# Kernel tuning notes

Measured on AMD Instinct MI355X. Metric: run time of the kernel, lower is better.

Reference implementation:

```python
import jax, jax.numpy as jnp
import numpy as np

SEQ, BATCH, IN, HID, LAYERS = 512, 32, 1024, 1024, 4


def setup_inputs() -> dict:
    key = jax.random.key(0)
    ks = jax.random.split(key, 5)
    s = 1.0 / np.sqrt(HID)  # torch-style U(-1/sqrt(H), 1/sqrt(H)) scale via scaled normal
    x = jax.random.normal(ks[0], (SEQ, BATCH, IN), dtype=jnp.float32)
    W_ih = jax.random.uniform(ks[1], (LAYERS, 4 * HID, IN), jnp.float32, -s, s)
    W_hh = jax.random.uniform(ks[2], (LAYERS, 4 * HID, HID), jnp.float32, -s, s)
    b_ih = jax.random.uniform(ks[3], (LAYERS, 4 * HID), jnp.float32, -s, s)
    b_hh = jax.random.uniform(ks[4], (LAYERS, 4 * HID), jnp.float32, -s, s)
    return {"x": x, "W_ih": W_ih, "W_hh": W_hh, "b_ih": b_ih, "b_hh": b_hh}


def _run_layer(inp, wih, whh, bih, bhh):
    # inp: [S, B, D]; wih: [4H, D]; whh: [4H, H]
    H = whh.shape[-1]
    B = inp.shape[1]
    # Precompute input projections for all timesteps in one big GEMM.
    x_gates = jnp.einsum('sbd,gd->sbg', inp, wih) + bih + bhh  # [S, B, 4H]

    def step(carry, xg_t):
        h, c = carry
        g = xg_t + h @ whh.T  # [B, 4H]
        i, f, gg, o = jnp.split(g, 4, axis=-1)  # torch gate order: i, f, g, o
        c_new = jax.nn.sigmoid(f) * c + jax.nn.sigmoid(i) * jnp.tanh(gg)
        h_new = jax.nn.sigmoid(o) * jnp.tanh(c_new)
        return (h_new, c_new), h_new

    h0 = jnp.zeros((B, H), inp.dtype)
    (h_last, c_last), ys = jax.lax.scan(step, (h0, h0), x_gates)
    return ys, h_last, c_last


def reference(x, W_ih, W_hh, b_ih, b_hh):
    out = x
    hs, cs = [], []
    for l in range(W_ih.shape[0]):  # fixed small layer count
        out, h, c = _run_layer(out, W_ih[l], W_hh[l], b_ih[l], b_hh[l])
        hs.append(h)
        cs.append(c)
    # x_outs: [S, B, H]; hs/cs: [L, B, H] (concatenation of per-layer final states)
    return out, jnp.stack(hs, axis=0), jnp.stack(cs, axis=0)
```

## Files before the change

kernel.cpp:

```cpp
#include <hip/hip_runtime.h>
#include <stdint.h>


#define SEQ    512
#define BATCH  32
#define HID    1024
#define G4     4096
#define LAYERS 4

typedef unsigned short u16;
typedef unsigned int u32;
typedef unsigned long long u64;
typedef __attribute__((ext_vector_type(8))) short bf8;
typedef __attribute__((ext_vector_type(4))) float f4;

__device__ __forceinline__ u16 f2bf(float f) {
  uint32_t u = __float_as_uint(f);
  u += 0x7FFFu + ((u >> 16) & 1u);
  return (u16)(u >> 16);
}
__device__ __forceinline__ float bf2f(u16 h) {
  return __uint_as_float(((uint32_t)h) << 16);
}
__device__ __forceinline__ float sigf(float x) { return 1.f / (1.f + __expf(-x)); }

__device__ __forceinline__ bf8 ld_bf8_sc(const u16* p) {
  union { u64 q[2]; bf8 v; } u;
  const u64* qp = (const u64*)p;
  u.q[0] = __hip_atomic_load(qp,     __ATOMIC_RELAXED, __HIP_MEMORY_SCOPE_AGENT);
  u.q[1] = __hip_atomic_load(qp + 1, __ATOMIC_RELAXED, __HIP_MEMORY_SCOPE_AGENT);
  return u.v;
}

__global__ void cvt_split_kernel(const float* __restrict__ in, u16* __restrict__ hi,
                                 u16* __restrict__ lo, int n4) {
  int i = blockIdx.x * 256 + threadIdx.x;
  if (i >= n4) return;
  float4 v = reinterpret_cast<const float4*>(in)[i];
  ushort4 h, l;
  h.x = f2bf(v.x); l.x = f2bf(v.x - bf2f(h.x));
  h.y = f2bf(v.y); l.y = f2bf(v.y - bf2f(h.y));
  h.z = f2bf(v.z); l.z = f2bf(v.z - bf2f(h.z));
  h.w = f2bf(v.w); l.w = f2bf(v.w - bf2f(h.w));
  reinterpret_cast<ushort4*>(hi)[i] = h;
  reinterpret_cast<ushort4*>(lo)[i] = l;
}

__global__ void bias_comb_kernel(const float* __restrict__ a, const float* __restrict__ b,
                                 float* __restrict__ o, int n) {
  int i = blockIdx.x * 256 + threadIdx.x;
  if (i < n) o[i] = a[i] + b[i];
}

__launch_bounds__(256)
__global__ void gemm_xproj(const u16* __restrict__ Ah, const u16* __restrict__ Al,
                           const u16* __restrict__ Bh, const u16* __restrict__ Bl,
                           const float* __restrict__ bias, float* __restrict__ C) {
  __shared__ u16 Ash[128 * 32];
  __shared__ u16 Asl[128 * 32];
  __shared__ u16 Bsh[128 * 32];
  __shared__ u16 Bsl[128 * 32];
  const int tid  = threadIdx.x;
  const int lane = tid & 63;
  const int w    = tid >> 6;
  const int wm   = (w >> 1) * 64, wn = (w & 1) * 64;
  const int m0   = blockIdx.x * 128, n0 = blockIdx.y * 128;
  const int fr   = lane & 15;
  const int fk   = (lane >> 4) * 8;
  const f4 fz = {0.f, 0.f, 0.f, 0.f};
  f4 acc[4][4];
#pragma unroll
  for (int i = 0; i < 4; ++i)
#pragma unroll
    for (int j = 0; j < 4; ++j) acc[i][j] = fz;

  for (int kt = 0; kt < 1024; kt += 32) {
    __syncthreads();
#pragma unroll
    for (int i = 0; i < 2; ++i) {
      const int e   = (i * 256 + tid) * 8;
      const int row = e >> 5, kc = e & 31;
      const int ldsbase = (i * 256 + (tid & 192)) * 8;
      const size_t goffA = (size_t)(m0 + row) * 1024 + kt + kc;
      const size_t goffB = (size_t)(n0 + row) * 1024 + kt + kc;
      __builtin_amdgcn_global_load_lds(
          (const __attribute__((address_space(1))) void*)(Ah + goffA),
          (__attribute__((address_space(3))) void*)(Ash + ldsbase), 16, 0, 0);
      __builtin_amdgcn_global_load_lds(
          (const __attribute__((address_space(1))) void*)(Al + goffA),
          (__attribute__((address_space(3))) void*)(Asl + ldsbase), 16, 0, 0);
      __builtin_amdgcn_global_load_lds(
          (const __attribute__((address_space(1))) void*)(Bh + goffB),
          (__attribute__((address_space(3))) void*)(Bsh + ldsbase), 16, 0, 0);
      __builtin_amdgcn_global_load_lds(
          (const __attribute__((address_space(1))) void*)(Bl + goffB),
          (__attribute__((address_space(3))) void*)(Bsl + ldsbase), 16, 0, 0);
    }
    __syncthreads();
    bf8 ah[4], al[4], bh[4], bl[4];
#pragma unroll
    for (int f = 0; f < 4; ++f) {
      ah[f] = *reinterpret_cast<const bf8*>(Ash + (wm + f * 16 + fr) * 32 + fk);
      al[f] = *reinterpret_cast<const bf8*>(Asl + (wm + f * 16 + fr) * 32 + fk);
      bh[f] = *reinterpret_cast<const bf8*>(Bsh + (wn + f * 16 + fr) * 32 + fk);
      bl[f] = *reinterpret_cast<const bf8*>(Bsl + (wn + f * 16 + fr) * 32 + fk);
    }
#pragma unroll
    for (int i = 0; i < 4; ++i)
#pragma unroll
      for (int j = 0; j < 4; ++j) {
        acc[i][j] = __builtin_amdgcn_mfma_f32_16x16x32_bf16(ah[i], bh[j], acc[i][j], 0, 0, 0);
        acc[i][j] = __builtin_amdgcn_mfma_f32_16x16x32_bf16(ah[i], bl[j], acc[i][j], 0, 0, 0);
        acc[i][j] = __builtin_amdgcn_mfma_f32_16x16x32_bf16(al[i], bh[j], acc[i][j], 0, 0, 0);
      }
  }
  const int cr0 = (lane >> 4) * 4;
#pragma unroll
  for (int i = 0; i < 4; ++i)
#pragma unroll
    for (int j = 0; j < 4; ++j)
#pragma unroll
      for (int q = 0; q < 4; ++q) {
        const int rr = m0 + wm + i * 16 + cr0 + q;
        const int cc = n0 + wn + j * 16 + fr;
        C[(size_t)rr * 4096 + cc] = acc[i][j][q] + bias[cc];
      }
}

#define WLD   1032
#define HPP_Q 32768
#define WBYTES (32 * WLD * 2)
#define SSMEM (2 * WBYTES + 16384)

__launch_bounds__(256, 1)
__global__ void lstm_scan(const float* __restrict__ gates,
                          const u16* __restrict__ Whh_hi,
                          const u16* __restrict__ Whh_lo,
                          u16* __restrict__ h_pp,
                          float* __restrict__ c_glob,
                          float* __restrict__ hseq_f,
                          float* __restrict__ hs_out,
                          float* __restrict__ cs_out,
                          int* __restrict__ slots,
                          int* __restrict__ go_rep,
                          int t0, int tag0, int nsteps, int is_last) {
  extern __shared__ char smem[];
  u16*   Wh  = (u16*)smem;
  u16*   Wl  = (u16*)(smem + WBYTES);
  float* red = (float*)(smem + 2 * WBYTES);

  const int bid = blockIdx.x;
  const int ug  = bid;
  const int tid = threadIdx.x, lane = tid & 63, w = tid >> 6;

  {
    const int n  = tid & 31;
    const int ch = tid >> 5;
    const size_t grow = (size_t)((n >> 3) * 1024 + ug * 8 + (n & 7));
    const u16* sh = Whh_hi + grow * 1024 + ch * 128;
    const u16* sl = Whh_lo + grow * 1024 + ch * 128;
    u16* dh = Wh + n * WLD + ch * 128;
    u16* dl = Wl + n * WLD + ch * 128;
#pragma unroll
    for (int it = 0; it < 16; ++it) {
      *reinterpret_cast<bf8*>(dh + it * 8) = *reinterpret_cast<const bf8*>(sh + it * 8);
      *reinterpret_cast<bf8*>(dl + it * 8) = *reinterpret_cast<const bf8*>(sl + it * 8);
    }
  }

  float c0 = 0.f, c1 = 0.f;
  int b = 0, up = 0, u0 = 0;
  if (tid < 128) {
    b = tid >> 2; up = tid & 3;
    u0 = ug * 8 + up * 2;
    c0 = c_glob[b * 1024 + u0];
    c1 = c_glob[b * 1024 + u0 + 1];
  }
  __syncthreads();

  const int fr = lane & 15, q4 = lane >> 4;
  const int khq = w;
  const int aeo0 = fr * 8;
  const int aeo1 = (16 + fr) * 8;
  const int brow0 = fr * WLD;
  const int brow1 = (16 + fr) * WLD;
  const int bcol0 = khq * 256 + q4 * 8;

  const f4 fz = {0.f, 0.f, 0.f, 0.f};

  for (int s = 0; s < nsteps; ++s) {
    const int t = t0 + s;
    float2 gp0, gp1, gp2, gp3;
    if (tid < 128) {
      const float* gr = gates + (size_t)(s * 32 + b) * 4096 + u0;
      gp0 = *(const float2*)(gr);
      gp1 = *(const float2*)(gr + 1024);
      gp2 = *(const float2*)(gr + 2048);
      gp3 = *(const float2*)(gr + 3072);
    }
    {
      const u16* hh = h_pp + (size_t)((t & 1) * 2 + 0) * HPP_Q;
      const u16* hl = h_pp + (size_t)((t & 1) * 2 + 1) * HPP_Q;
      f4 a00 = fz, a01 = fz, a10 = fz, a11 = fz;
#pragma unroll
      for (int kc8 = 0; kc8 < 32; kc8 += 4) {
        const int ab = (khq * 32 + kc8 + q4) * 256;
        bf8 avh0 = ld_bf8_sc(hh + ab + aeo0);
        bf8 avl0 = ld_bf8_sc(hl + ab + aeo0);
        bf8 avh1 = ld_bf8_sc(hh + ab + aeo1);
        bf8 avl1 = ld_bf8_sc(hl + ab + aeo1);
        const int bc = bcol0 + kc8 * 8;
        bf8 bvh0 = *reinterpret_cast<const bf8*>(Wh + brow0 + bc);
        bf8 bvl0 = *reinterpret_cast<const bf8*>(Wl + brow0 + bc);
        bf8 bvh1 = *reinterpret_cast<const bf8*>(Wh + brow1 + bc);
        bf8 bvl1 = *reinterpret_cast<const bf8*>(Wl + brow1 + bc);
        a00 = __builtin_amdgcn_mfma_f32_16x16x32_bf16(avh0, bvh0, a00, 0, 0, 0);
        a00 = __builtin_amdgcn_mfma_f32_16x16x32_bf16(avh0, bvl0, a00, 0, 0, 0);
        a00 = __builtin_amdgcn_mfma_f32_16x16x32_bf16(avl0, bvh0, a00, 0, 0, 0);
        a01 = __builtin_amdgcn_mfma_f32_16x16x32_bf16(avh0, bvh1, a01, 0, 0, 0);
        a01 = __builtin_amdgcn_mfma_f32_16x16x32_bf16(avh0, bvl1, a01, 0, 0, 0);
        a01 = __builtin_amdgcn_mfma_f32_16x16x32_bf16(avl0, bvh1, a01, 0, 0, 0);
        a10 = __builtin_amdgcn_mfma_f32_16x16x32_bf16(avh1, bvh0, a10, 0, 0, 0);
        a10 = __builtin_amdgcn_mfma_f32_16x16x32_bf16(avh1, bvl0, a10, 0, 0, 0);
        a10 = __builtin_amdgcn_mfma_f32_16x16x32_bf16(avl1, bvh0, a10, 0, 0, 0);
        a11 = __builtin_amdgcn_mfma_f32_16x16x32_bf16(avh1, bvh1, a11, 0, 0, 0);
        a11 = __builtin_amdgcn_mfma_f32_16x16x32_bf16(avh1, bvl1, a11, 0, 0, 0);
        a11 = __builtin_amdgcn_mfma_f32_16x16x32_bf16(avl1, bvh1, a11, 0, 0, 0);
      }
      float* r00 = red + (khq * 2 + 0) * 512 + fr * 16 + q4 * 4;
      float* r01 = r00 + 256;
      float* r10 = red + (khq * 2 + 1) * 512 + fr * 16 + q4 * 4;
      float* r11 = r10 + 256;
#pragma unroll
      for (int q = 0; q < 4; ++q) {
        r00[q] = a00[q]; r01[q] = a01[q]; r10[q] = a10[q]; r11[q] = a11[q];
      }
    }
    __syncthreads();
    if (tid < 128) {
      const int bl = b & 15, bmt = b >> 4;
      float g00, g01, g02, g03, g10, g11, g12, g13;
      {
        const int nb0 = (up * 2) * 16 + bl;
        float s0, s1, s2, s3;
#pragma unroll
        for (int j = 0; j < 2; ++j) {
          const int nb = nb0 + j * 16;
          s0 = s1 = s2 = s3 = 0.f;
#pragma unroll
          for (int kq = 0; kq < 4; ++kq) {
            const float* rb = red + (kq * 2 + bmt) * 512 + nb;
            s0 += rb[0 * 128];
            s1 += rb[1 * 128];
            s2 += rb[2 * 128];
            s3 += rb[3 * 128];
          }
          if (j == 0) { g00 = s0 + gp0.x; g01 = s1 + gp1.x; g02 = s2 + gp2.x; g03 = s3 + gp3.x; }
          else        { g10 = s0 + gp0.y; g11 = s1 + gp1.y; g12 = s2 + gp2.y; g13 = s3 + gp3.y; }
        }
      }
      const float i0 = sigf(g00), f0 = sigf(g01), z0 = tanhf(g02), o0 = sigf(g03);
      c0 = f0 * c0 + i0 * z0;
      const float h0 = o0 * tanhf(c0);
      const float i1 = sigf(g10), f1 = sigf(g11), z1 = tanhf(g12), o1 = sigf(g13);
      c1 = f1 * c1 + i1 * z1;
      const float h1 = o1 * tanhf(c1);
      const u64 hv = ((u64)__float_as_uint(h1) << 32) | (u64)__float_as_uint(h0);
      __hip_atomic_store((u64*)(hseq_f + ((size_t)t * 32 + b) * 1024 + u0), hv,
                         __ATOMIC_RELAXED, __HIP_MEMORY_SCOPE_AGENT);
      const u16 h0h = f2bf(h0), h0l = f2bf(h0 - bf2f(h0h));
      const u16 h1h = f2bf(h1), h1l = f2bf(h1 - bf2f(h1h));
      const int par2 = ((t + 1) & 1) * 2;
      const int tix  = ug * 256 + b * 8 + up * 2;
      __hip_atomic_store((u32*)(h_pp + (size_t)par2 * HPP_Q + tix),
                         (u32)h0h | ((u32)h1h << 16),
                         __ATOMIC_RELAXED, __HIP_MEMORY_SCOPE_AGENT);
      __hip_atomic_store((u32*)(h_pp + (size_t)(par2 + 1) * HPP_Q + tix),
                         (u32)h0l | ((u32)h1l << 16),
                         __ATOMIC_RELAXED, __HIP_MEMORY_SCOPE_AGENT);
      if (is_last && s == nsteps - 1) {
        hs_out[b * 1024 + u0]     = h0;
        hs_out[b * 1024 + u0 + 1] = h1;
        cs_out[b * 1024 + u0]     = c0;
        cs_out[b * 1024 + u0 + 1] = c1;
      }
    }
    __syncthreads();
    const int tag = tag0 + s + 1;
    if (tid == 0)
      __hip_atomic_store(slots + bid, tag, __ATOMIC_RELEASE, __HIP_MEMORY_SCOPE_AGENT);
    if (bid == 0) {
      if (w == 0) {
        for (;;) {
          int v0 = __hip_atomic_load(slots + lane,      __ATOMIC_RELAXED, __HIP_MEMORY_SCOPE_AGENT);
          int v1 = __hip_atomic_load(slots + 64 + lane, __ATOMIC_RELAXED, __HIP_MEMORY_SCOPE_AGENT);
          if (__all(v0 >= tag && v1 >= tag)) break;
          __builtin_amdgcn_s_sleep(1);
        }
        __builtin_amdgcn_fence(__ATOMIC_ACQ_REL, "agent");
        if (lane < 32)
          __hip_atomic_store(go_rep + lane * 16, tag, __ATOMIC_RELAXED, __HIP_MEMORY_SCOPE_AGENT);
      }
    } else if (tid == 0) {
      while (__hip_atomic_load(go_rep + (bid & 31) * 16, __ATOMIC_RELAXED, __HIP_MEMORY_SCOPE_AGENT) < tag)
        __builtin_amdgcn_s_sleep(2);
    }
    __syncthreads();
  }
  if (tid < 128) {
    c_glob[b * 1024 + u0]     = c0;
    c_glob[b * 1024 + u0 + 1] = c1;
  }
}

extern "C" void kernel_launch(void* const* d_in, const int* in_sizes, int n_in,
                              void* d_out, int out_size, void* d_ws, size_t ws_size,
                              hipStream_t stream) {
  const float* x   = (const float*)d_in[0];
  const float* Wih = (const float*)d_in[1];
  const float* Whh = (const float*)d_in[2];
  const float* bih = (const float*)d_in[3];
  const float* bhh = (const float*)d_in[4];
  float* out = (float*)d_out;

  float* outh = out;
  const size_t OFF1 = (size_t)SEQ * BATCH * HID;
  const size_t OFF2 = OFF1 + (size_t)LAYERS * BATCH * HID;

  char* ws = (char*)d_ws;
  u16*   wih_hi = (u16*)ws;
  u16*   wih_lo = (u16*)(ws + (8ull  << 20));
  u16*   whh_hi = (u16*)(ws + (16ull << 20));
  u16*   whh_lo = (u16*)(ws + (24ull << 20));
  float* biasc  = (float*)(ws + (32ull << 20));
  u16*   h_pp   = (u16*)(ws + (32ull << 20) + (64ull << 10));
  float* c_glob = (float*)(ws + (32ull << 20) + (320ull << 10));
  int*   bar    = (int*)(ws + (32ull << 20) + (448ull << 10));
  char*  dynws  = ws + (33ull << 20);

  int T = 128;
  while (T > 8 && (33ull << 20) + (size_t)T * (640ull << 10) > ws_size) T >>= 1;
  const int nchunk = SEQ / T;
  u16*   xb_hi = (u16*)dynws;
  u16*   xb_lo = (u16*)(dynws + (size_t)T * BATCH * HID * sizeof(u16));
  float* gates = (float*)(dynws + (size_t)2 * T * BATCH * HID * sizeof(u16));

  hipFuncSetAttribute(reinterpret_cast<const void*>(lstm_scan),
                      hipFuncAttributeMaxDynamicSharedMemorySize, SSMEM);

  hipMemsetAsync(bar, 0, 4096, stream);
  bias_comb_kernel<<<(LAYERS * G4 + 255) / 256, 256, 0, stream>>>(bih, bhh, biasc, LAYERS * G4);

  int tag0 = 0;
  for (int l = 0; l < LAYERS; ++l) {
    cvt_split_kernel<<<G4 * HID / 4 / 256, 256, 0, stream>>>(
        Wih + (size_t)l * G4 * HID, wih_hi, wih_lo, G4 * HID / 4);
    cvt_split_kernel<<<G4 * HID / 4 / 256, 256, 0, stream>>>(
        Whh + (size_t)l * G4 * HID, whh_hi, whh_lo, G4 * HID / 4);
    hipMemsetAsync(h_pp, 0, 4 * HPP_Q * sizeof(u16), stream);
    hipMemsetAsync(c_glob, 0, BATCH * HID * sizeof(float), stream);
    for (int cch = 0; cch < nchunk; ++cch) {
      const float* asrc = (l == 0) ? (x + (size_t)cch * T * BATCH * HID)
                                   : (outh + (size_t)cch * T * BATCH * HID);
      cvt_split_kernel<<<T * BATCH * HID / 4 / 256, 256, 0, stream>>>(
          asrc, xb_hi, xb_lo, T * BATCH * HID / 4);
      gemm_xproj<<<dim3(T * BATCH / 128, 32), 256, 0, stream>>>(
          xb_hi, xb_lo, wih_hi, wih_lo, biasc + l * G4, gates);
      lstm_scan<<<128, 256, SSMEM, stream>>>(
          gates, whh_hi, whh_lo, h_pp, c_glob,
          outh,
          out + OFF1 + (size_t)l * BATCH * HID,
          out + OFF2 + (size_t)l * BATCH * HID,
          bar, bar + 128,
          cch * T, tag0, T, (cch == nchunk - 1) ? 1 : 0);
      tag0 += T;
    }
  }
  (void)in_sizes; (void)n_in; (void)out_size;
}
```

Measured before the change: 14.75 ms.

## Keep recurrent weights in registers and replace two-level grid barrier with all-to-all polling

The W_hh slice for each block now sits in VGPRs instead of LDS, which removes the per-step LDS weight reads and the large dynamic shared allocation. The grid barrier becomes a flat scheme: each wave publishes its own slot, and every wave polls all 512 slots directly, so the master-block relay through go_rep is gone. Gate inputs for the next step are prefetched during the current step, and tanhf is replaced with an exp-based approximation. The risks are higher register pressure, more polling traffic to L2 from every wave, and tanh accuracy that may drift for extreme inputs.

```diff
diff --git a/kernel.cpp b/kernel.cpp
--- a/kernel.cpp
+++ b/kernel.cpp
@@ -23,6 +23,9 @@
   return __uint_as_float(((uint32_t)h) << 16);
 }
 __device__ __forceinline__ float sigf(float x) { return 1.f / (1.f + __expf(-x)); }
+__device__ __forceinline__ float tanhfast(float x) {
+  return 1.f - 2.f / (1.f + __expf(2.f * x));
+}
 
 __device__ __forceinline__ bf8 ld_bf8_sc(const u16* p) {
   union { u64 q[2]; bf8 v; } u;
@@ -127,10 +130,7 @@
       }
 }
 
-#define WLD   1032
 #define HPP_Q 32768
-#define WBYTES (32 * WLD * 2)
-#define SSMEM (2 * WBYTES + 16384)
 
 __launch_bounds__(256, 1)
 __global__ void lstm_scan(const float* __restrict__ gates,
@@ -142,90 +142,78 @@
                           float* __restrict__ hs_out,
                           float* __restrict__ cs_out,
                           int* __restrict__ slots,
-                          int* __restrict__ go_rep,
                           int t0, int tag0, int nsteps, int is_last) {
-  extern __shared__ char smem[];
-  u16*   Wh  = (u16*)smem;
-  u16*   Wl  = (u16*)(smem + WBYTES);
-  float* red = (float*)(smem + 2 * WBYTES);
+  __shared__ float red[4096];
 
   const int bid = blockIdx.x;
   const int ug  = bid;
   const int tid = threadIdx.x, lane = tid & 63, w = tid >> 6;
 
+  const int fr = lane & 15, q4 = lane >> 4;
+  const int khq = w;
+  const int bcol0 = khq * 256 + q4 * 8;
+
+  bf8 wh0[8], wl0[8], wh1[8], wl1[8];
   {
-    const int n  = tid & 31;
-    const int ch = tid >> 5;
-    const size_t grow = (size_t)((n >> 3) * 1024 + ug * 8 + (n & 7));
-    const u16* sh = Whh_hi + grow * 1024 + ch * 128;
-    const u16* sl = Whh_lo + grow * 1024 + ch * 128;
-    u16* dh = Wh + n * WLD + ch * 128;
-    u16* dl = Wl + n * WLD + ch * 128;
-#pragma unroll
-    for (int it = 0; it < 16; ++it) {
-      *reinterpret_cast<bf8*>(dh + it * 8) = *reinterpret_cast<const bf8*>(sh + it * 8);
-      *reinterpret_cast<bf8*>(dl + it * 8) = *reinterpret_cast<const bf8*>(sl + it * 8);
+    const size_t grow0 = (size_t)((fr >> 3) * 1024 + ug * 8 + (fr & 7));
+    const size_t grow1 = grow0 + 2048;
+    const u16* bh0 = Whh_hi + grow0 * 1024 + bcol0;
+    const u16* bl0 = Whh_lo + grow0 * 1024 + bcol0;
+    const u16* bh1 = Whh_hi + grow1 * 1024 + bcol0;
+    const u16* bl1 = Whh_lo + grow1 * 1024 + bcol0;
+#pragma unroll
+    for (int i = 0; i < 8; ++i) {
+      wh0[i] = *reinterpret_cast<const bf8*>(bh0 + 32 * i);
+      wl0[i] = *reinterpret_cast<const bf8*>(bl0 + 32 * i);
+      wh1[i] = *reinterpret_cast<const bf8*>(bh1 + 32 * i);
+      wl1[i] = *reinterpret_cast<const bf8*>(bl1 + 32 * i);
     }
   }
 
   float c0 = 0.f, c1 = 0.f;
   int b = 0, up = 0, u0 = 0;
+  float2 gp0, gp1, gp2, gp3;
   if (tid < 128) {
     b = tid >> 2; up = tid & 3;
     u0 = ug * 8 + up * 2;
     c0 = c_glob[b * 1024 + u0];
     c1 = c_glob[b * 1024 + u0 + 1];
-  }
-  __syncthreads();
-
-  const int fr = lane & 15, q4 = lane >> 4;
-  const int khq = w;
+    const float* gr = gates + (size_t)b * 4096 + u0;
+    gp0 = *(const float2*)(gr);
+    gp1 = *(const float2*)(gr + 1024);
+    gp2 = *(const float2*)(gr + 2048);
+    gp3 = *(const float2*)(gr + 3072);
+  }
+
   const int aeo0 = fr * 8;
   const int aeo1 = (16 + fr) * 8;
-  const int brow0 = fr * WLD;
-  const int brow1 = (16 + fr) * WLD;
-  const int bcol0 = khq * 256 + q4 * 8;
-
   const f4 fz = {0.f, 0.f, 0.f, 0.f};
 
   for (int s = 0; s < nsteps; ++s) {
     const int t = t0 + s;
-    float2 gp0, gp1, gp2, gp3;
-    if (tid < 128) {
-      const float* gr = gates + (size_t)(s * 32 + b) * 4096 + u0;
-      gp0 = *(const float2*)(gr);
-      gp1 = *(const float2*)(gr + 1024);
-      gp2 = *(const float2*)(gr + 2048);
-      gp3 = *(const float2*)(gr + 3072);
-    }
     {
       const u16* hh = h_pp + (size_t)((t & 1) * 2 + 0) * HPP_Q;
       const u16* hl = h_pp + (size_t)((t & 1) * 2 + 1) * HPP_Q;
       f4 a00 = fz, a01 = fz, a10 = fz, a11 = fz;
 #pragma unroll
-      for (int kc8 = 0; kc8 < 32; kc8 += 4) {
-        const int ab = (khq * 32 + kc8 + q4) * 256;
+      for (int i = 0; i < 8; ++i) {
+        const int ab = (khq * 32 + 4 * i + q4) * 256;
         bf8 avh0 = ld_bf8_sc(hh + ab + aeo0);
         bf8 avl0 = ld_bf8_sc(hl + ab + aeo0);
         bf8 avh1 = ld_bf8_sc(hh + ab + aeo1);
         bf8 avl1 = ld_bf8_sc(hl + ab + aeo1);
-        const int bc = bcol0 + kc8 * 8;
-        bf8 bvh0 = *reinterpret_cast<const bf8*>(Wh + brow0 + bc);
-        bf8 bvl0 = *reinterpret_cast<const bf8*>(Wl + brow0 + bc);
-        bf8 bvh1 = *reinterpret_cast<const bf8*>(Wh + brow1 + bc);
-        bf8 bvl1 = *reinterpret_cast<const bf8*>(Wl + brow1 + bc);
-        a00 = __builtin_amdgcn_mfma_f32_16x16x32_bf16(avh0, bvh0, a00, 0, 0, 0);
-        a00 = __builtin_amdgcn_mfma_f32_16x16x32_bf16(avh0, bvl0, a00, 0, 0, 0);
-        a00 = __builtin_amdgcn_mfma_f32_16x16x32_bf16(avl0, bvh0, a00, 0, 0, 0);
-        a01 = __builtin_amdgcn_mfma_f32_16x16x32_bf16(avh0, bvh1, a01, 0, 0, 0);
-        a01 = __builtin_amdgcn_mfma_f32_16x16x32_bf16(avh0, bvl1, a01, 0, 0, 0);
-        a01 = __builtin_amdgcn_mfma_f32_16x16x32_bf16(avl0, bvh1, a01, 0, 0, 0);
-        a10 = __builtin_amdgcn_mfma_f32_16x16x32_bf16(avh1, bvh0, a10, 0, 0, 0);
-        a10 = __builtin_amdgcn_mfma_f32_16x16x32_bf16(avh1, bvl0, a10, 0, 0, 0);
-        a10 = __builtin_amdgcn_mfma_f32_16x16x32_bf16(avl1, bvh0, a10, 0, 0, 0);
-        a11 = __builtin_amdgcn_mfma_f32_16x16x32_bf16(avh1, bvh1, a11, 0, 0, 0);
-        a11 = __builtin_amdgcn_mfma_f32_16x16x32_bf16(avh1, bvl1, a11, 0, 0, 0);
-        a11 = __builtin_amdgcn_mfma_f32_16x16x32_bf16(avl1, bvh1, a11, 0, 0, 0);
+        a00 = __builtin_amdgcn_mfma_f32_16x16x32_bf16(avh0, wh0[i], a00, 0, 0, 0);
+        a00 = __builtin_amdgcn_mfma_f32_16x16x32_bf16(avh0, wl0[i], a00, 0, 0, 0);
+        a00 = __builtin_amdgcn_mfma_f32_16x16x32_bf16(avl0, wh0[i], a00, 0, 0, 0);
+        a01 = __builtin_amdgcn_mfma_f32_16x16x32_bf16(avh0, wh1[i], a01, 0, 0, 0);
+        a01 = __builtin_amdgcn_mfma_f32_16x16x32_bf16(avh0, wl1[i], a01, 0, 0, 0);
+        a01 = __builtin_amdgcn_mfma_f32_16x16x32_bf16(avl0, wh1[i], a01, 0, 0, 0);
+        a10 = __builtin_amdgcn_mfma_f32_16x16x32_bf16(avh1, wh0[i], a10, 0, 0, 0);
+        a10 = __builtin_amdgcn_mfma_f32_16x16x32_bf16(avh1, wl0[i], a10, 0, 0, 0);
+        a10 = __builtin_amdgcn_mfma_f32_16x16x32_bf16(avl1, wh0[i], a10, 0, 0, 0);
+        a11 = __builtin_amdgcn_mfma_f32_16x16x32_bf16(avh1, wh1[i], a11, 0, 0, 0);
+        a11 = __builtin_amdgcn_mfma_f32_16x16x32_bf16(avh1, wl1[i], a11, 0, 0, 0);
+        a11 = __builtin_amdgcn_mfma_f32_16x16x32_bf16(avl1, wh1[i], a11, 0, 0, 0);
       }
       float* r00 = red + (khq * 2 + 0) * 512 + fr * 16 + q4 * 4;
       float* r01 = r00 + 256;
@@ -238,6 +226,15 @@
     }
     __syncthreads();
     if (tid < 128) {
+      float2 gn0, gn1, gn2, gn3;
+      {
+        const int sp = (s + 1 < nsteps) ? s + 1 : s;
+        const float* gr = gates + (size_t)(sp * 32 + b) * 4096 + u0;
+        gn0 = *(const float2*)(gr);
+        gn1 = *(const float2*)(gr + 1024);
+        gn2 = *(const float2*)(gr + 2048);
+        gn3 = *(const float2*)(gr + 3072);
+      }
       const int bl = b & 15, bmt = b >> 4;
       float g00, g01, g02, g03, g10, g11, g12, g13;
       {
@@ -259,12 +256,12 @@
           else        { g10 = s0 + gp0.y; g11 = s1 + gp1.y; g12 = s2 + gp2.y; g13 = s3 + gp3.y; }
         }
       }
-      const float i0 = sigf(g00), f0 = sigf(g01), z0 = tanhf(g02), o0 = sigf(g03);
+      const float i0 = sigf(g00), f0 = sigf(g01), z0 = tanhfast(g02), o0 = sigf(g03);
       c0 = f0 * c0 + i0 * z0;
-      const float h0 = o0 * tanhf(c0);
-      const float i1 = sigf(g10), f1 = sigf(g11), z1 = tanhf(g12), o1 = sigf(g13);
+      const float h0 = o0 * tanhfast(c0);
+      const float i1 = sigf(g10), f1 = sigf(g11), z1 = tanhfast(g12), o1 = sigf(g13);
       c1 = f1 * c1 + i1 * z1;
-      const float h1 = o1 * tanhf(c1);
+      const float h1 = o1 * tanhfast(c1);
       const u64 hv = ((u64)__float_as_uint(h1) << 32) | (u64)__float_as_uint(h0);
       __hip_atomic_store((u64*)(hseq_f + ((size_t)t * 32 + b) * 1024 + u0), hv,
                          __ATOMIC_RELAXED, __HIP_MEMORY_SCOPE_AGENT);
@@ -284,28 +281,28 @@
         cs_out[b * 1024 + u0]     = c0;
         cs_out[b * 1024 + u0 + 1] = c1;
       }
-    }
-    __syncthreads();
-    const int tag = tag0 + s + 1;
-    if (tid == 0)
-      __hip_atomic_store(slots + bid, tag, __ATOMIC_RELEASE, __HIP_MEMORY_SCOPE_AGENT);
-    if (bid == 0) {
-      if (w == 0) {
-        for (;;) {
-          int v0 = __hip_atomic_load(slots + lane,      __ATOMIC_RELAXED, __HIP_MEMORY_SCOPE_AGENT);
-          int v1 = __hip_atomic_load(slots + 64 + lane, __ATOMIC_RELAXED, __HIP_MEMORY_SCOPE_AGENT);
-          if (__all(v0 >= tag && v1 >= tag)) break;
-          __builtin_amdgcn_s_sleep(1);
-        }
-        __builtin_amdgcn_fence(__ATOMIC_ACQ_REL, "agent");
-        if (lane < 32)
-          __hip_atomic_store(go_rep + lane * 16, tag, __ATOMIC_RELAXED, __HIP_MEMORY_SCOPE_AGENT);
-      }
-    } else if (tid == 0) {
-      while (__hip_atomic_load(go_rep + (bid & 31) * 16, __ATOMIC_RELAXED, __HIP_MEMORY_SCOPE_AGENT) < tag)
-        __builtin_amdgcn_s_sleep(2);
-    }
-    __syncthreads();
+      gp0 = gn0; gp1 = gn1; gp2 = gn2; gp3 = gn3;
+    }
+    if (s + 1 < nsteps) {
+      const int tag = tag0 + s + 1;
+      if (w < 2) asm volatile("s_waitcnt vmcnt(0)" ::: "memory");
+      if (lane == 0)
+        __hip_atomic_store(slots + bid * 4 + w, tag, __ATOMIC_RELAXED, __HIP_MEMORY_SCOPE_AGENT);
+      const u64* sl64 = (const u64*)slots;
+      for (;;) {
+        u64 v0 = __hip_atomic_load(sl64 + lane * 4 + 0, __ATOMIC_RELAXED, __HIP_MEMORY_SCOPE_AGENT);
+        u64 v1 = __hip_atomic_load(sl64 + lane * 4 + 1, __ATOMIC_RELAXED, __HIP_MEMORY_SCOPE_AGENT);
+        u64 v2 = __hip_atomic_load(sl64 + lane * 4 + 2, __ATOMIC_RELAXED, __HIP_MEMORY_SCOPE_AGENT);
+        u64 v3 = __hip_atomic_load(sl64 + lane * 4 + 3, __ATOMIC_RELAXED, __HIP_MEMORY_SCOPE_AGENT);
+        bool ok = ((int)v0 >= tag) && ((int)(v0 >> 32) >= tag)
+               && ((int)v1 >= tag) && ((int)(v1 >> 32) >= tag)
+               && ((int)v2 >= tag) && ((int)(v2 >> 32) >= tag)
+               && ((int)v3 >= tag) && ((int)(v3 >> 32) >= tag);
+        if (__all(ok)) break;
+        __builtin_amdgcn_s_sleep(1);
+      }
+      __builtin_amdgcn_sched_barrier(0);
+    }
   }
   if (tid < 128) {
     c_glob[b * 1024 + u0]     = c0;
@@ -344,9 +341,6 @@
   u16*   xb_hi = (u16*)dynws;
   u16*   xb_lo = (u16*)(dynws + (size_t)T * BATCH * HID * sizeof(u16));
   float* gates = (float*)(dynws + (size_t)2 * T * BATCH * HID * sizeof(u16));
-
-  hipFuncSetAttribute(reinterpret_cast<const void*>(lstm_scan),
-                      hipFuncAttributeMaxDynamicSharedMemorySize, SSMEM);
 
   hipMemsetAsync(bar, 0, 4096, stream);
   bias_comb_kernel<<<(LAYERS * G4 + 255) / 256, 256, 0, stream>>>(bih, bhh, biasc, LAYERS * G4);
@@ -366,12 +360,12 @@
           asrc, xb_hi, xb_lo, T * BATCH * HID / 4);
       gemm_xproj<<<dim3(T * BATCH / 128, 32), 256, 0, stream>>>(
           xb_hi, xb_lo, wih_hi, wih_lo, biasc + l * G4, gates);
-      lstm_scan<<<128, 256, SSMEM, stream>>>(
+      lstm_scan<<<128, 256, 0, stream>>>(
           gates, whh_hi, whh_lo, h_pp, c_glob,
           outh,
           out + OFF1 + (size_t)l * BATCH * HID,
           out + OFF2 + (size_t)l * BATCH * HID,
-          bar, bar + 128,
+          bar,
           cch * T, tag0, T, (cch == nchunk - 1) ? 1 : 0);
       tag0 += T;
     }
```

Result: slower. 22.79 ms (+54.6%).

## Replace centralized grid barrier with per-wave polling of producer flags

Applied to the files above, without the earlier changes.

Drops the two-stage grid barrier (all blocks report to block 0, which then broadcasts a go flag). Instead each block publishes a per-step flag in its own padded slot, and each wave spins only on the 8×4 producer blocks whose h slice it reads, right before its MFMA k-range. This aims to cut barrier round-trip latency on the sequential time loop and lets blocks drift apart slightly. Flags are now stored relaxed rather than with release ordering, and double-buffered h may be overwritten early, so there is a memory-ordering and WAR risk. Also swaps tanhf for an exp-based fast tanh and changes the LDS row padding of the weight tile.

```diff
diff --git a/kernel.cpp b/kernel.cpp
--- a/kernel.cpp
+++ b/kernel.cpp
@@ -23,6 +23,9 @@
   return __uint_as_float(((uint32_t)h) << 16);
 }
 __device__ __forceinline__ float sigf(float x) { return 1.f / (1.f + __expf(-x)); }
+__device__ __forceinline__ float tanhfast(float x) {
+  return 1.f - 2.f / (1.f + __expf(2.f * x));
+}
 
 __device__ __forceinline__ bf8 ld_bf8_sc(const u16* p) {
   union { u64 q[2]; bf8 v; } u;
@@ -127,7 +130,7 @@
       }
 }
 
-#define WLD   1032
+#define WLD   1036
 #define HPP_Q 32768
 #define WBYTES (32 * WLD * 2)
 #define SSMEM (2 * WBYTES + 16384)
@@ -142,7 +145,6 @@
                           float* __restrict__ hs_out,
                           float* __restrict__ cs_out,
                           int* __restrict__ slots,
-                          int* __restrict__ go_rep,
                           int t0, int tag0, int nsteps, int is_last) {
   extern __shared__ char smem[];
   u16*   Wh  = (u16*)smem;
@@ -185,7 +187,7 @@
   const int brow0 = fr * WLD;
   const int brow1 = (16 + fr) * WLD;
   const int bcol0 = khq * 256 + q4 * 8;
-
+  const int pbase = (khq * 32 + q4) * 16;
   const f4 fz = {0.f, 0.f, 0.f, 0.f};
 
   for (int s = 0; s < nsteps; ++s) {
@@ -197,6 +199,21 @@
       gp1 = *(const float2*)(gr + 1024);
       gp2 = *(const float2*)(gr + 2048);
       gp3 = *(const float2*)(gr + 3072);
+    }
+    {
+      const int tagS = tag0 + s;
+      for (;;) {
+        bool ok = true;
+#pragma unroll
+        for (int i = 0; i < 8; ++i) {
+          int v = __hip_atomic_load(slots + pbase + i * 64,
+                                    __ATOMIC_RELAXED, __HIP_MEMORY_SCOPE_AGENT);
+          ok &= (v >= tagS);
+        }
+        if (ok) break;
+        __builtin_amdgcn_s_sleep(1);
+      }
+      __builtin_amdgcn_sched_barrier(0);
     }
     {
       const u16* hh = h_pp + (size_t)((t & 1) * 2 + 0) * HPP_Q;
@@ -259,12 +276,12 @@
           else        { g10 = s0 + gp0.y; g11 = s1 + gp1.y; g12 = s2 + gp2.y; g13 = s3 + gp3.y; }
         }
       }
-      const float i0 = sigf(g00), f0 = sigf(g01), z0 = tanhf(g02), o0 = sigf(g03);
+      const float i0 = sigf(g00), f0 = sigf(g01), z0 = tanhfast(g02), o0 = sigf(g03);
       c0 = f0 * c0 + i0 * z0;
-      const float h0 = o0 * tanhf(c0);
-      const float i1 = sigf(g10), f1 = sigf(g11), z1 = tanhf(g12), o1 = sigf(g13);
+      const float h0 = o0 * tanhfast(c0);
+      const float i1 = sigf(g10), f1 = sigf(g11), z1 = tanhfast(g12), o1 = sigf(g13);
       c1 = f1 * c1 + i1 * z1;
-      const float h1 = o1 * tanhf(c1);
+      const float h1 = o1 * tanhfast(c1);
       const u64 hv = ((u64)__float_as_uint(h1) << 32) | (u64)__float_as_uint(h0);
       __hip_atomic_store((u64*)(hseq_f + ((size_t)t * 32 + b) * 1024 + u0), hv,
                          __ATOMIC_RELAXED, __HIP_MEMORY_SCOPE_AGENT);
@@ -286,26 +303,9 @@
       }
     }
     __syncthreads();
-    const int tag = tag0 + s + 1;
     if (tid == 0)
-      __hip_atomic_store(slots + bid, tag, __ATOMIC_RELEASE, __HIP_MEMORY_SCOPE_AGENT);
-    if (bid == 0) {
-      if (w == 0) {
-        for (;;) {
-          int v0 = __hip_atomic_load(slots + lane,      __ATOMIC_RELAXED, __HIP_MEMORY_SCOPE_AGENT);
-          int v1 = __hip_atomic_load(slots + 64 + lane, __ATOMIC_RELAXED, __HIP_MEMORY_SCOPE_AGENT);
-          if (__all(v0 >= tag && v1 >= tag)) break;
-          __builtin_amdgcn_s_sleep(1);
-        }
-        __builtin_amdgcn_fence(__ATOMIC_ACQ_REL, "agent");
-        if (lane < 32)
-          __hip_atomic_store(go_rep + lane * 16, tag, __ATOMIC_RELAXED, __HIP_MEMORY_SCOPE_AGENT);
-      }
-    } else if (tid == 0) {
-      while (__hip_atomic_load(go_rep + (bid & 31) * 16, __ATOMIC_RELAXED, __HIP_MEMORY_SCOPE_AGENT) < tag)
-        __builtin_amdgcn_s_sleep(2);
-    }
-    __syncthreads();
+      __hip_atomic_store(slots + bid * 16, tag0 + s + 1,
+                         __ATOMIC_RELAXED, __HIP_MEMORY_SCOPE_AGENT);
   }
   if (tid < 128) {
     c_glob[b * 1024 + u0]     = c0;
@@ -348,7 +348,7 @@
   hipFuncSetAttribute(reinterpret_cast<const void*>(lstm_scan),
                       hipFuncAttributeMaxDynamicSharedMemorySize, SSMEM);
 
-  hipMemsetAsync(bar, 0, 4096, stream);
+  hipMemsetAsync(bar, 0, 8192, stream);
   bias_comb_kernel<<<(LAYERS * G4 + 255) / 256, 256, 0, stream>>>(bih, bhh, biasc, LAYERS * G4);
 
   int tag0 = 0;
@@ -371,7 +371,7 @@
           outh,
           out + OFF1 + (size_t)l * BATCH * HID,
           out + OFF2 + (size_t)l * BATCH * HID,
-          bar, bar + 128,
+          bar,
           cch * T, tag0, T, (cch == nchunk - 1) ? 1 : 0);
       tag0 += T;
     }
```

Result: faster. 13.74 ms (-6.8%).
